# Optimization experiments

Hardware: AMD Instinct MI355X
Metric: run time of the kernel (lower is better)

The kernel has to match this reference:

```python
import jax, jax.numpy as jnp
import numpy as np

H = 128  # hidden_size
I = 28   # input_size
C = 10   # num_classes


def setup_inputs() -> dict:
    key = jax.random.key(0)
    ks = jax.random.split(key, 11)
    s = 1.0 / np.sqrt(H)  # torch nn.RNN init scale
    return {
        "x": jax.random.normal(ks[0], (8192, 28, I), dtype=jnp.float32),
        "W_ih0": jax.random.uniform(ks[1], (H, I), jnp.float32, -s, s),
        "W_hh0": jax.random.uniform(ks[2], (H, H), jnp.float32, -s, s),
        "b_ih0": jax.random.uniform(ks[3], (H,), jnp.float32, -s, s),
        "b_hh0": jax.random.uniform(ks[4], (H,), jnp.float32, -s, s),
        "W_ih1": jax.random.uniform(ks[5], (H, H), jnp.float32, -s, s),
        "W_hh1": jax.random.uniform(ks[6], (H, H), jnp.float32, -s, s),
        "b_ih1": jax.random.uniform(ks[7], (H,), jnp.float32, -s, s),
        "b_hh1": jax.random.uniform(ks[8], (H,), jnp.float32, -s, s),
        "fc_w": jax.random.uniform(ks[9], (C, H), jnp.float32, -s, s),
        "fc_b": jax.random.uniform(ks[10], (C,), jnp.float32, -s, s),
    }


def _rnn_layer_full(x, W_ih, b_ih, W_hh, b_hh):
    # x: [B, T, D] -> full output sequence [B, T, H]
    B = x.shape[0]
    h0 = jnp.zeros((B, H), x.dtype)
    xw = jnp.einsum('btd,hd->bth', x, W_ih) + b_ih  # precompute input GEMM

    def step(h, xw_t):
        h = jnp.tanh(xw_t + h @ W_hh.T + b_hh)
        return h, h

    _, ys = jax.lax.scan(step, h0, jnp.swapaxes(xw, 0, 1))  # [T, B, H]
    return jnp.swapaxes(ys, 0, 1)


def _rnn_layer_last(x, W_ih, b_ih, W_hh, b_hh):
    # only the final hidden state is needed downstream
    B = x.shape[0]
    h0 = jnp.zeros((B, H), x.dtype)
    xw = jnp.einsum('btd,hd->bth', x, W_ih) + b_ih

    def step(h, xw_t):
        h = jnp.tanh(xw_t + h @ W_hh.T + b_hh)
        return h, None

    h_last, _ = jax.lax.scan(step, h0, jnp.swapaxes(xw, 0, 1))
    return h_last


def reference(x, W_ih0, W_hh0, b_ih0, b_hh0, W_ih1, W_hh1, b_ih1, b_hh1, fc_w, fc_b):
    out0 = _rnn_layer_full(x, W_ih0, b_ih0, W_hh0, b_hh0)   # [B, T, H]
    h_last = _rnn_layer_last(out0, W_ih1, b_ih1, W_hh1, b_hh1)  # [B, H] == out[:, -1, :]
    return h_last @ fc_w.T + fc_b  # [B, C]
```

## Files before the change

kernel.cpp:

```cpp
#include <hip/hip_runtime.h>

#define HSZ 128
#define ISZ 28
#define TSZ 28
#define CSZ 10
#define BT  16
#define NT  256
#define HP  136
#define XP  40

typedef _Float16 half_t;
typedef _Float16 v8h __attribute__((ext_vector_type(8)));
typedef _Float16 v4h __attribute__((ext_vector_type(4)));
typedef float v4f __attribute__((ext_vector_type(4)));

__device__ __forceinline__ float fast_tanh(float x) {
    float e = __expf(2.f * x);
    return 1.f - 2.f * __builtin_amdgcn_rcpf(e + 1.f);
}

__global__ __launch_bounds__(NT, 2)
void rnn_mfma2(const float* __restrict__ x,
               const float* __restrict__ W_ih0, const float* __restrict__ W_hh0,
               const float* __restrict__ b_ih0, const float* __restrict__ b_hh0,
               const float* __restrict__ W_ih1, const float* __restrict__ W_hh1,
               const float* __restrict__ b_ih1, const float* __restrict__ b_hh1,
               const float* __restrict__ fc_w, const float* __restrict__ fc_b,
               float* __restrict__ out)
{
    __shared__ half_t h0s[2][BT * HP];
    __shared__ half_t h1s[2][BT * HP];
    __shared__ half_t xss[2][BT * XP];

    const int tid  = threadIdx.x;
    const int wave = tid >> 6;
    const int lane = tid & 63;
    const int ln   = lane & 15;
    const int quad = lane >> 4;
    const int kq   = quad * 8;
    const int b0   = blockIdx.x * BT;

    v8h aWx[2];
    v8h aW0[2][4];
    v8h aW1i[2][4];
    v8h aW1h[2][4];
    v4f bias0[2], bias1[2];

#pragma unroll
    for (int nt = 0; nt < 2; ++nt) {
        const int base = (wave * 2 + nt) * 16;
        const int row  = base + ln;
#pragma unroll
        for (int r = 0; r < 4; ++r) {
            const int c = base + quad * 4 + r;
            bias0[nt][r] = b_ih0[c] + b_hh0[c];
            bias1[nt][r] = b_ih1[c] + b_hh1[c];
        }
#pragma unroll
        for (int j = 0; j < 8; ++j) {
            const int k = kq + j;
            aWx[nt][j] = (half_t)(k < ISZ ? W_ih0[row * ISZ + k] : 0.f);
        }
#pragma unroll
        for (int ks = 0; ks < 4; ++ks) {
            const float4* p0 = (const float4*)(W_hh0 + row * HSZ + ks * 32 + kq);
            const float4* p1 = (const float4*)(W_ih1 + row * HSZ + ks * 32 + kq);
            const float4* p2 = (const float4*)(W_hh1 + row * HSZ + ks * 32 + kq);
            float4 a = p0[0], b = p0[1];
            aW0[nt][ks] = (v8h){(half_t)a.x, (half_t)a.y, (half_t)a.z, (half_t)a.w,
                                (half_t)b.x, (half_t)b.y, (half_t)b.z, (half_t)b.w};
            a = p1[0]; b = p1[1];
            aW1i[nt][ks] = (v8h){(half_t)a.x, (half_t)a.y, (half_t)a.z, (half_t)a.w,
                                 (half_t)b.x, (half_t)b.y, (half_t)b.z, (half_t)b.w};
            a = p2[0]; b = p2[1];
            aW1h[nt][ks] = (v8h){(half_t)a.x, (half_t)a.y, (half_t)a.z, (half_t)a.w,
                                 (half_t)b.x, (half_t)b.y, (half_t)b.z, (half_t)b.w};
        }
    }

    for (int idx = tid; idx < BT * XP; idx += NT) {
        xss[0][idx] = (half_t)0.f;
        xss[1][idx] = (half_t)0.f;
    }
    for (int idx = tid; idx < BT * HP; idx += NT)
        h1s[0][idx] = (half_t)0.f;
    __syncthreads();
    for (int idx = tid; idx < BT * ISZ; idx += NT) {
        const int m = idx / ISZ, i = idx - m * ISZ;
        const float* xr = x + (size_t)(b0 + m) * (TSZ * ISZ);
        xss[0][m * XP + i] = (half_t)xr[i];
        xss[1][m * XP + i] = (half_t)(ISZ + i < 2 * ISZ ? xr[ISZ + i] : 0.f);
    }
    __syncthreads();

    {
        const v8h bx = *(const v8h*)&xss[0][ln * XP + kq];
        v4f a0[2] = {bias0[0], bias0[1]};
#pragma unroll
        for (int nt = 0; nt < 2; ++nt)
            a0[nt] = __builtin_amdgcn_mfma_f32_16x16x32_f16(aWx[nt], bx, a0[nt], 0, 0, 0);
#pragma unroll
        for (int nt = 0; nt < 2; ++nt) {
            const int base = (wave * 2 + nt) * 16;
            v4h p = {(half_t)fast_tanh(a0[nt][0]), (half_t)fast_tanh(a0[nt][1]),
                     (half_t)fast_tanh(a0[nt][2]), (half_t)fast_tanh(a0[nt][3])};
            *(v4h*)&h0s[0][ln * HP + base + quad * 4] = p;
        }
    }
    __syncthreads();

    for (int t = 0; t < TSZ - 1; ++t) {
        const int pr = t & 1;

        if (t < TSZ - 2) {
            for (int idx = tid; idx < BT * ISZ; idx += NT) {
                const int m = idx / ISZ, i = idx - m * ISZ;
                xss[pr][m * XP + i] =
                    (half_t)x[(size_t)(b0 + m) * (TSZ * ISZ) + (t + 2) * ISZ + i];
            }
        }

        v8h bh0[4], bh1[4];
#pragma unroll
        for (int ks = 0; ks < 4; ++ks) {
            bh0[ks] = *(const v8h*)&h0s[pr][ln * HP + ks * 32 + kq];
            bh1[ks] = *(const v8h*)&h1s[pr][ln * HP + ks * 32 + kq];
        }
        const v8h bx = *(const v8h*)&xss[pr ^ 1][ln * XP + kq];

        v4f a1[2] = {bias1[0], bias1[1]};
        v4f a0[2] = {bias0[0], bias0[1]};
#pragma unroll
        for (int nt = 0; nt < 2; ++nt)
            a0[nt] = __builtin_amdgcn_mfma_f32_16x16x32_f16(aWx[nt], bx, a0[nt], 0, 0, 0);
#pragma unroll
        for (int ks = 0; ks < 4; ++ks) {
#pragma unroll
            for (int nt = 0; nt < 2; ++nt) {
                a1[nt] = __builtin_amdgcn_mfma_f32_16x16x32_f16(aW1i[nt][ks], bh0[ks], a1[nt], 0, 0, 0);
                a1[nt] = __builtin_amdgcn_mfma_f32_16x16x32_f16(aW1h[nt][ks], bh1[ks], a1[nt], 0, 0, 0);
                a0[nt] = __builtin_amdgcn_mfma_f32_16x16x32_f16(aW0[nt][ks], bh0[ks], a0[nt], 0, 0, 0);
            }
        }

#pragma unroll
        for (int nt = 0; nt < 2; ++nt) {
            const int base = (wave * 2 + nt) * 16;
            v4h p1 = {(half_t)fast_tanh(a1[nt][0]), (half_t)fast_tanh(a1[nt][1]),
                      (half_t)fast_tanh(a1[nt][2]), (half_t)fast_tanh(a1[nt][3])};
            *(v4h*)&h1s[pr ^ 1][ln * HP + base + quad * 4] = p1;
            v4h p0 = {(half_t)fast_tanh(a0[nt][0]), (half_t)fast_tanh(a0[nt][1]),
                      (half_t)fast_tanh(a0[nt][2]), (half_t)fast_tanh(a0[nt][3])};
            *(v4h*)&h0s[pr ^ 1][ln * HP + base + quad * 4] = p0;
        }
        __syncthreads();
    }

    {
        const int pr = (TSZ - 1) & 1;
        v8h bh0[4], bh1[4];
#pragma unroll
        for (int ks = 0; ks < 4; ++ks) {
            bh0[ks] = *(const v8h*)&h0s[pr][ln * HP + ks * 32 + kq];
            bh1[ks] = *(const v8h*)&h1s[pr][ln * HP + ks * 32 + kq];
        }
        v4f a1[2] = {bias1[0], bias1[1]};
#pragma unroll
        for (int ks = 0; ks < 4; ++ks) {
#pragma unroll
            for (int nt = 0; nt < 2; ++nt) {
                a1[nt] = __builtin_amdgcn_mfma_f32_16x16x32_f16(aW1i[nt][ks], bh0[ks], a1[nt], 0, 0, 0);
                a1[nt] = __builtin_amdgcn_mfma_f32_16x16x32_f16(aW1h[nt][ks], bh1[ks], a1[nt], 0, 0, 0);
            }
        }
#pragma unroll
        for (int nt = 0; nt < 2; ++nt) {
            const int base = (wave * 2 + nt) * 16;
            v4h p1 = {(half_t)fast_tanh(a1[nt][0]), (half_t)fast_tanh(a1[nt][1]),
                      (half_t)fast_tanh(a1[nt][2]), (half_t)fast_tanh(a1[nt][3])};
            *(v4h*)&h1s[pr ^ 1][ln * HP + base + quad * 4] = p1;
        }
        __syncthreads();
    }

    if (tid < BT * CSZ) {
        const int m = tid / CSZ, cc = tid - m * CSZ;
        float s = fc_b[cc];
#pragma unroll
        for (int k8 = 0; k8 < HSZ / 8; ++k8) {
            const v8h hv = *(const v8h*)&h1s[0][m * HP + k8 * 8];
            const float4 w0 = *(const float4*)(fc_w + cc * HSZ + k8 * 8);
            const float4 w1 = *(const float4*)(fc_w + cc * HSZ + k8 * 8 + 4);
            s += (float)hv[0] * w0.x + (float)hv[1] * w0.y +
                 (float)hv[2] * w0.z + (float)hv[3] * w0.w +
                 (float)hv[4] * w1.x + (float)hv[5] * w1.y +
                 (float)hv[6] * w1.z + (float)hv[7] * w1.w;
        }
        out[(b0 + m) * CSZ + cc] = s;
    }
}

extern "C" void kernel_launch(void* const* d_in, const int* in_sizes, int n_in,
                              void* d_out, int out_size, void* d_ws, size_t ws_size,
                              hipStream_t stream) {
    const float* x     = (const float*)d_in[0];
    const float* W_ih0 = (const float*)d_in[1];
    const float* W_hh0 = (const float*)d_in[2];
    const float* b_ih0 = (const float*)d_in[3];
    const float* b_hh0 = (const float*)d_in[4];
    const float* W_ih1 = (const float*)d_in[5];
    const float* W_hh1 = (const float*)d_in[6];
    const float* b_ih1 = (const float*)d_in[7];
    const float* b_hh1 = (const float*)d_in[8];
    const float* fc_w  = (const float*)d_in[9];
    const float* fc_b  = (const float*)d_in[10];
    float* out = (float*)d_out;

    const int B = in_sizes[0] / (TSZ * ISZ);
    dim3 grid(B / BT), block(NT);
    rnn_mfma2<<<grid, block, 0, stream>>>(x, W_ih0, W_hh0, b_ih0, b_hh0,
                                          W_ih1, W_hh1, b_ih1, b_hh1,
                                          fc_w, fc_b, out);
}
```

Before: 140.2 us.

## Use eight waves with one output tile each and register-prefetch x one step ahead

```diff
diff --git a/kernel.cpp b/kernel.cpp
--- a/kernel.cpp
+++ b/kernel.cpp
@@ -5,9 +5,9 @@
 #define TSZ 28
 #define CSZ 10
 #define BT  16
-#define NT  256
+#define NT  512
 #define HP  136
-#define XP  40
+#define XP  32
 
 typedef _Float16 half_t;
 typedef _Float16 v8h __attribute__((ext_vector_type(8)));
@@ -19,8 +19,8 @@
     return 1.f - 2.f * __builtin_amdgcn_rcpf(e + 1.f);
 }
 
-__global__ __launch_bounds__(NT, 2)
-void rnn_mfma2(const float* __restrict__ x,
+__global__ __launch_bounds__(NT, 4)
+void rnn_mfma3(const float* __restrict__ x,
                const float* __restrict__ W_ih0, const float* __restrict__ W_hh0,
                const float* __restrict__ b_ih0, const float* __restrict__ b_hh0,
                const float* __restrict__ W_ih1, const float* __restrict__ W_hh1,
@@ -39,149 +39,118 @@
     const int quad = lane >> 4;
     const int kq   = quad * 8;
     const int b0   = blockIdx.x * BT;
+    const int base = wave * 16;
+    const int row  = base + ln;
 
-    v8h aWx[2];
-    v8h aW0[2][4];
-    v8h aW1i[2][4];
-    v8h aW1h[2][4];
-    v4f bias0[2], bias1[2];
-
+    v8h aWx, aW0[4], aW1i[4], aW1h[4];
+    v4f bias0, bias1;
+    {
+        float4 p = *(const float4*)(b_ih0 + base + quad * 4);
+        float4 q = *(const float4*)(b_hh0 + base + quad * 4);
+        bias0 = (v4f){p.x + q.x, p.y + q.y, p.z + q.z, p.w + q.w};
+        p = *(const float4*)(b_ih1 + base + quad * 4);
+        q = *(const float4*)(b_hh1 + base + quad * 4);
+        bias1 = (v4f){p.x + q.x, p.y + q.y, p.z + q.z, p.w + q.w};
+    }
+    {
+        const float* pw = W_ih0 + row * ISZ + kq;
+        float4 a = *(const float4*)pw;
+        float4 b = (kq < 24) ? *(const float4*)(pw + 4) : make_float4(0.f, 0.f, 0.f, 0.f);
+        aWx = (v8h){(half_t)a.x, (half_t)a.y, (half_t)a.z, (half_t)a.w,
+                    (half_t)b.x, (half_t)b.y, (half_t)b.z, (half_t)b.w};
+    }
 #pragma unroll
-    for (int nt = 0; nt < 2; ++nt) {
-        const int base = (wave * 2 + nt) * 16;
-        const int row  = base + ln;
-#pragma unroll
-        for (int r = 0; r < 4; ++r) {
-            const int c = base + quad * 4 + r;
-            bias0[nt][r] = b_ih0[c] + b_hh0[c];
-            bias1[nt][r] = b_ih1[c] + b_hh1[c];
-        }
-#pragma unroll
-        for (int j = 0; j < 8; ++j) {
-            const int k = kq + j;
-            aWx[nt][j] = (half_t)(k < ISZ ? W_ih0[row * ISZ + k] : 0.f);
-        }
-#pragma unroll
-        for (int ks = 0; ks < 4; ++ks) {
-            const float4* p0 = (const float4*)(W_hh0 + row * HSZ + ks * 32 + kq);
-            const float4* p1 = (const float4*)(W_ih1 + row * HSZ + ks * 32 + kq);
-            const float4* p2 = (const float4*)(W_hh1 + row * HSZ + ks * 32 + kq);
-            float4 a = p0[0], b = p0[1];
-            aW0[nt][ks] = (v8h){(half_t)a.x, (half_t)a.y, (half_t)a.z, (half_t)a.w,
-                                (half_t)b.x, (half_t)b.y, (half_t)b.z, (half_t)b.w};
-            a = p1[0]; b = p1[1];
-            aW1i[nt][ks] = (v8h){(half_t)a.x, (half_t)a.y, (half_t)a.z, (half_t)a.w,
-                                 (half_t)b.x, (half_t)b.y, (half_t)b.z, (half_t)b.w};
-            a = p2[0]; b = p2[1];
-            aW1h[nt][ks] = (v8h){(half_t)a.x, (half_t)a.y, (half_t)a.z, (half_t)a.w,
-                                 (half_t)b.x, (half_t)b.y, (half_t)b.z, (half_t)b.w};
-        }
+    for (int ks = 0; ks < 4; ++ks) {
+        const float4* p0 = (const float4*)(W_hh0 + row * HSZ + ks * 32 + kq);
+        const float4* p1 = (const float4*)(W_ih1 + row * HSZ + ks * 32 + kq);
+        const float4* p2 = (const float4*)(W_hh1 + row * HSZ + ks * 32 + kq);
+        float4 a = p0[0], b = p0[1];
+        aW0[ks] = (v8h){(half_t)a.x, (half_t)a.y, (half_t)a.z, (half_t)a.w,
+                        (half_t)b.x, (half_t)b.y, (half_t)b.z, (half_t)b.w};
+        a = p1[0]; b = p1[1];
+        aW1i[ks] = (v8h){(half_t)a.x, (half_t)a.y, (half_t)a.z, (half_t)a.w,
+                         (half_t)b.x, (half_t)b.y, (half_t)b.z, (half_t)b.w};
+        a = p2[0]; b = p2[1];
+        aW1h[ks] = (v8h){(half_t)a.x, (half_t)a.y, (half_t)a.z, (half_t)a.w,
+                         (half_t)b.x, (half_t)b.y, (half_t)b.z, (half_t)b.w};
     }
 
-    for (int idx = tid; idx < BT * XP; idx += NT) {
-        xss[0][idx] = (half_t)0.f;
-        xss[1][idx] = (half_t)0.f;
-    }
+    const int  xm  = tid >> 5;
+    const int  xi  = tid & 31;
+    const bool xok = xi < ISZ;
+    const float* xrow = x + (size_t)(b0 + xm) * (TSZ * ISZ) + xi;
+
+    xss[0][xm * XP + xi] = (half_t)(xok ? xrow[0] : 0.f);
+    xss[1][xm * XP + xi] = (half_t)(xok ? xrow[ISZ] : 0.f);
+    float xcur = xok ? xrow[2 * ISZ] : 0.f;
+
     for (int idx = tid; idx < BT * HP; idx += NT)
         h1s[0][idx] = (half_t)0.f;
-    __syncthreads();
-    for (int idx = tid; idx < BT * ISZ; idx += NT) {
-        const int m = idx / ISZ, i = idx - m * ISZ;
-        const float* xr = x + (size_t)(b0 + m) * (TSZ * ISZ);
-        xss[0][m * XP + i] = (half_t)xr[i];
-        xss[1][m * XP + i] = (half_t)(ISZ + i < 2 * ISZ ? xr[ISZ + i] : 0.f);
-    }
     __syncthreads();
 
     {
         const v8h bx = *(const v8h*)&xss[0][ln * XP + kq];
-        v4f a0[2] = {bias0[0], bias0[1]};
-#pragma unroll
-        for (int nt = 0; nt < 2; ++nt)
-            a0[nt] = __builtin_amdgcn_mfma_f32_16x16x32_f16(aWx[nt], bx, a0[nt], 0, 0, 0);
-#pragma unroll
-        for (int nt = 0; nt < 2; ++nt) {
-            const int base = (wave * 2 + nt) * 16;
-            v4h p = {(half_t)fast_tanh(a0[nt][0]), (half_t)fast_tanh(a0[nt][1]),
-                     (half_t)fast_tanh(a0[nt][2]), (half_t)fast_tanh(a0[nt][3])};
-            *(v4h*)&h0s[0][ln * HP + base + quad * 4] = p;
-        }
+        v4f a0 = bias0;
+        a0 = __builtin_amdgcn_mfma_f32_16x16x32_f16(aWx, bx, a0, 0, 0, 0);
+        v4h p = {(half_t)fast_tanh(a0[0]), (half_t)fast_tanh(a0[1]),
+                 (half_t)fast_tanh(a0[2]), (half_t)fast_tanh(a0[3])};
+        *(v4h*)&h0s[0][ln * HP + base + quad * 4] = p;
     }
     __syncthreads();
 
     for (int t = 0; t < TSZ - 1; ++t) {
         const int pr = t & 1;
 
-        if (t < TSZ - 2) {
-            for (int idx = tid; idx < BT * ISZ; idx += NT) {
-                const int m = idx / ISZ, i = idx - m * ISZ;
-                xss[pr][m * XP + i] =
-                    (half_t)x[(size_t)(b0 + m) * (TSZ * ISZ) + (t + 2) * ISZ + i];
-            }
+        float xnew = 0.f;
+        if (t < TSZ - 3 && xok) xnew = xrow[(t + 3) * ISZ];
+
+        v8h bh0[4];
+#pragma unroll
+        for (int ks = 0; ks < 4; ++ks)
+            bh0[ks] = *(const v8h*)&h0s[pr][ln * HP + ks * 32 + kq];
+        const v8h bx = *(const v8h*)&xss[pr ^ 1][ln * XP + kq];
+
+        v4f a1 = bias1, a0 = bias0;
+        a0 = __builtin_amdgcn_mfma_f32_16x16x32_f16(aWx, bx, a0, 0, 0, 0);
+#pragma unroll
+        for (int ks = 0; ks < 4; ++ks) {
+            const v8h bh1 = *(const v8h*)&h1s[pr][ln * HP + ks * 32 + kq];
+            a1 = __builtin_amdgcn_mfma_f32_16x16x32_f16(aW1i[ks], bh0[ks], a1, 0, 0, 0);
+            a1 = __builtin_amdgcn_mfma_f32_16x16x32_f16(aW1h[ks], bh1,     a1, 0, 0, 0);
+            a0 = __builtin_amdgcn_mfma_f32_16x16x32_f16(aW0[ks],  bh0[ks], a0, 0, 0, 0);
         }
 
-        v8h bh0[4], bh1[4];
-#pragma unroll
-        for (int ks = 0; ks < 4; ++ks) {
-            bh0[ks] = *(const v8h*)&h0s[pr][ln * HP + ks * 32 + kq];
-            bh1[ks] = *(const v8h*)&h1s[pr][ln * HP + ks * 32 + kq];
-        }
-        const v8h bx = *(const v8h*)&xss[pr ^ 1][ln * XP + kq];
-
-        v4f a1[2] = {bias1[0], bias1[1]};
-        v4f a0[2] = {bias0[0], bias0[1]};
-#pragma unroll
-        for (int nt = 0; nt < 2; ++nt)
-            a0[nt] = __builtin_amdgcn_mfma_f32_16x16x32_f16(aWx[nt], bx, a0[nt], 0, 0, 0);
-#pragma unroll
-        for (int ks = 0; ks < 4; ++ks) {
-#pragma unroll
-            for (int nt = 0; nt < 2; ++nt) {
-                a1[nt] = __builtin_amdgcn_mfma_f32_16x16x32_f16(aW1i[nt][ks], bh0[ks], a1[nt], 0, 0, 0);
-                a1[nt] = __builtin_amdgcn_mfma_f32_16x16x32_f16(aW1h[nt][ks], bh1[ks], a1[nt], 0, 0, 0);
-                a0[nt] = __builtin_amdgcn_mfma_f32_16x16x32_f16(aW0[nt][ks], bh0[ks], a0[nt], 0, 0, 0);
-            }
+        {
+            v4h p1 = {(half_t)fast_tanh(a1[0]), (half_t)fast_tanh(a1[1]),
+                      (half_t)fast_tanh(a1[2]), (half_t)fast_tanh(a1[3])};
+            *(v4h*)&h1s[pr ^ 1][ln * HP + base + quad * 4] = p1;
+            v4h p0 = {(half_t)fast_tanh(a0[0]), (half_t)fast_tanh(a0[1]),
+                      (half_t)fast_tanh(a0[2]), (half_t)fast_tanh(a0[3])};
+            *(v4h*)&h0s[pr ^ 1][ln * HP + base + quad * 4] = p0;
         }
 
-#pragma unroll
-        for (int nt = 0; nt < 2; ++nt) {
-            const int base = (wave * 2 + nt) * 16;
-            v4h p1 = {(half_t)fast_tanh(a1[nt][0]), (half_t)fast_tanh(a1[nt][1]),
-                      (half_t)fast_tanh(a1[nt][2]), (half_t)fast_tanh(a1[nt][3])};
-            *(v4h*)&h1s[pr ^ 1][ln * HP + base + quad * 4] = p1;
-            v4h p0 = {(half_t)fast_tanh(a0[nt][0]), (half_t)fast_tanh(a0[nt][1]),
-                      (half_t)fast_tanh(a0[nt][2]), (half_t)fast_tanh(a0[nt][3])};
-            *(v4h*)&h0s[pr ^ 1][ln * HP + base + quad * 4] = p0;
-        }
+        if (t < TSZ - 2)
+            xss[pr][xm * XP + xi] = (half_t)xcur;
+        xcur = xnew;
+
         __syncthreads();
     }
 
     {
         const int pr = (TSZ - 1) & 1;
-        v8h bh0[4], bh1[4];
+        v4f a1 = bias1;
 #pragma unroll
         for (int ks = 0; ks < 4; ++ks) {
-            bh0[ks] = *(const v8h*)&h0s[pr][ln * HP + ks * 32 + kq];
-            bh1[ks] = *(const v8h*)&h1s[pr][ln * HP + ks * 32 + kq];
+            const v8h bh0 = *(const v8h*)&h0s[pr][ln * HP + ks * 32 + kq];
+            const v8h bh1 = *(const v8h*)&h1s[pr][ln * HP + ks * 32 + kq];
+            a1 = __builtin_amdgcn_mfma_f32_16x16x32_f16(aW1i[ks], bh0, a1, 0, 0, 0);
+            a1 = __builtin_amdgcn_mfma_f32_16x16x32_f16(aW1h[ks], bh1, a1, 0, 0, 0);
         }
-        v4f a1[2] = {bias1[0], bias1[1]};
-#pragma unroll
-        for (int ks = 0; ks < 4; ++ks) {
-#pragma unroll
-            for (int nt = 0; nt < 2; ++nt) {
-                a1[nt] = __builtin_amdgcn_mfma_f32_16x16x32_f16(aW1i[nt][ks], bh0[ks], a1[nt], 0, 0, 0);
-                a1[nt] = __builtin_amdgcn_mfma_f32_16x16x32_f16(aW1h[nt][ks], bh1[ks], a1[nt], 0, 0, 0);
-            }
-        }
-#pragma unroll
-        for (int nt = 0; nt < 2; ++nt) {
-            const int base = (wave * 2 + nt) * 16;
-            v4h p1 = {(half_t)fast_tanh(a1[nt][0]), (half_t)fast_tanh(a1[nt][1]),
-                      (half_t)fast_tanh(a1[nt][2]), (half_t)fast_tanh(a1[nt][3])};
-            *(v4h*)&h1s[pr ^ 1][ln * HP + base + quad * 4] = p1;
-        }
-        __syncthreads();
+        v4h p1 = {(half_t)fast_tanh(a1[0]), (half_t)fast_tanh(a1[1]),
+                  (half_t)fast_tanh(a1[2]), (half_t)fast_tanh(a1[3])};
+        *(v4h*)&h1s[pr ^ 1][ln * HP + base + quad * 4] = p1;
     }
+    __syncthreads();
 
     if (tid < BT * CSZ) {
         const int m = tid / CSZ, cc = tid - m * CSZ;
@@ -218,7 +187,7 @@
 
     const int B = in_sizes[0] / (TSZ * ISZ);
     dim3 grid(B / BT), block(NT);
-    rnn_mfma2<<<grid, block, 0, stream>>>(x, W_ih0, W_hh0, b_ih0, b_hh0,
+    rnn_mfma3<<<grid, block, 0, stream>>>(x, W_ih0, W_hh0, b_ih0, b_hh0,
                                           W_ih1, W_hh1, b_ih1, b_hh1,
                                           fc_w, fc_b, out);
 }
```

Result: faster. 127.3 us (-9.2%).
